# Performance work log

Measured on AMD Instinct MI355X. Metric: run time of the kernel, lower is better.

## Reference

```python
import jax, jax.numpy as jnp
import numpy as np

INPUT_DIM, HIDDEN_DIM, N_CLASSES = 512, 256, 2
TOP_RATIO, MIN_PATCHES, K_INST = 0.7, 128, 8
B, N = 4, 16384


def setup_inputs() -> dict:
    key = jax.random.key(0)
    ks = jax.random.split(key, 10)
    D, H, C = INPUT_DIM, HIDDEN_DIM, N_CLASSES
    s = lambda fan: 1.0 / np.sqrt(fan)
    return {
        "features": jax.random.normal(ks[0], (B, N, D), dtype=jnp.float32),
        # attention_net: Linear(D->H) (dropout is identity in eval)
        "Wa": jax.random.uniform(ks[1], (D, H), minval=-s(D), maxval=s(D), dtype=jnp.float32),
        "ba": jax.random.uniform(ks[2], (H,), minval=-s(D), maxval=s(D), dtype=jnp.float32),
        # per-class attention branches: Linear(H->1), stacked over classes
        "Wbr": jax.random.uniform(ks[3], (C, H), minval=-s(H), maxval=s(H), dtype=jnp.float32),
        "bbr": jax.random.uniform(ks[4], (C,), minval=-s(H), maxval=s(H), dtype=jnp.float32),
        # per-class instance classifiers: Linear(D->H) -> ReLU -> Linear(H->2)
        "W1": jax.random.uniform(ks[5], (C, D, H), minval=-s(D), maxval=s(D), dtype=jnp.float32),
        "b1": jax.random.uniform(ks[6], (C, H), minval=-s(D), maxval=s(D), dtype=jnp.float32),
        "W2": jax.random.uniform(ks[7], (C, H, 2), minval=-s(H), maxval=s(H), dtype=jnp.float32),
        "b2": jax.random.uniform(ks[8], (C, 2), minval=-s(H), maxval=s(H), dtype=jnp.float32),
    }


def reference(features, Wa, ba, Wbr, bbr, W1, b1, W2, b2):
    Bb, Nn, D = features.shape
    C = Wbr.shape[0]

    # ---- compute_attention ----
    h = jax.nn.relu(features @ Wa + ba)                       # (B,N,H)
    a_logits = jnp.einsum('bnh,ch->bcn', h, Wbr) + bbr[None, :, None]
    attn_all = jax.nn.softmax(a_logits, axis=-1)              # (B,C,N)
    combined = attn_all.mean(axis=1)                          # (B,N)

    # ---- per-sample top-k selection (k static under jit) ----
    k = min(max(int(Nn * TOP_RATIO), MIN_PATCHES), Nn)
    _, sel_idx = jax.lax.top_k(combined, k)                   # (B,k)
    sel_idx = jnp.sort(sel_idx, axis=-1)
    selected = jnp.take_along_axis(features, sel_idx[..., None], axis=1)  # (B,k,D)

    # ---- instance clustering loss (vectorized over B x C) ----
    kk = min(K_INST, Nn // 2)
    _, top_idx = jax.lax.top_k(attn_all, kk)                  # (B,C,kk)
    _, bot_idx = jax.lax.top_k(-attn_all, kk)                 # largest=False
    both_idx = jnp.concatenate([top_idx, bot_idx], axis=-1)   # (B,C,2kk)
    inst = features[jnp.arange(Bb)[:, None, None], both_idx]  # (B,C,2kk,D)
    h1 = jax.nn.relu(jnp.einsum('bckd,cdh->bckh', inst, W1) + b1[None, :, None, :])
    logits = jnp.einsum('bckh,cho->bcko', h1, W2) + b2[None, :, None, :]  # (B,C,2kk,2)
    labels = jnp.concatenate([jnp.ones(kk, jnp.int32), jnp.zeros(kk, jnp.int32)])
    logp = jax.nn.log_softmax(logits, axis=-1)
    ce = -jnp.take_along_axis(
        logp, jnp.broadcast_to(labels[None, None, :, None], (Bb, C, 2 * kk, 1)), axis=-1
    )[..., 0]                                                 # (B,C,2kk)
    cl_loss = ce.mean(axis=-1).sum() / (Bb * C)

    return selected, combined, sel_idx, cl_loss
```

## Files before the change

kernel.cpp:

```cpp
#include <hip/hip_runtime.h>

#define NB 4
#define NP 16384
#define DD 512
#define HH 256
#define CC 2
#define KSEL 11468
#define TOTP (NB*NP)
#define BCAP 4096

#define OFF_COMB (NB*KSEL*DD)
#define OFF_IDX  (OFF_COMB + NB*NP)
#define OFF_LOSS (OFF_IDX + NB*KSEL)

#define WS_ALOGIT 0
#define WS_ATTN   (NB*CC*NP)
#define WS_SELIDX (2*NB*CC*NP)
#define WS_MZ     (WS_SELIDX + NB*KSEL)
#define WS_BCNT   (WS_MZ + 16)
#define WS_BLIST  (WS_BCNT + 4)
#define WS_TOP16  (WS_BLIST + NB*BCAP)
#define WS_CE     (WS_TOP16 + 128)

typedef __attribute__((ext_vector_type(8))) short short8x;
typedef __attribute__((ext_vector_type(4))) float f32x4;

__device__ __forceinline__ unsigned short f2bf(float x){
  unsigned u = __float_as_uint(x);
  unsigned r = (u + 0x7FFFu + ((u >> 16) & 1u)) >> 16;
  return (unsigned short)r;
}

__global__ __launch_bounds__(256) void waconv_kernel(
    const float* __restrict__ Wa, unsigned short* __restrict__ WaT)
{
  __shared__ float tile[32][33];
  const int tx = threadIdx.x, ty = threadIdx.y;
  const int k0 = blockIdx.x * 32, n0 = blockIdx.y * 32;
  #pragma unroll
  for (int i=0;i<4;++i)
    tile[ty+8*i][tx] = Wa[(size_t)(k0+ty+8*i)*HH + n0 + tx];
  __syncthreads();
  #pragma unroll
  for (int i=0;i<4;++i)
    WaT[(size_t)(n0+ty+8*i)*DD + k0 + tx] = f2bf(tile[tx][ty+8*i]);
}

__global__ __launch_bounds__(512) void gemm_mfma_kernel(
    const float* __restrict__ feat, const unsigned short* __restrict__ WaT,
    const float* __restrict__ ba, const float* __restrict__ Wbr,
    const float* __restrict__ bbr, float* __restrict__ aL)
{
  __shared__ __attribute__((aligned(16))) unsigned char smem[65536];
  __shared__ float sBA[HH], sW0[HH], sW1[HH];
  unsigned char* sA = smem;
  unsigned char* sB = smem + 16384;

  const int tid  = threadIdx.x;
  const int lane = tid & 63;
  const int wid  = tid >> 6;
  const int wm = wid >> 2, wn = wid & 3;
  const int fr = lane & 15, fq = lane >> 4;
  const int p0 = blockIdx.x * 128;
  const float bb0 = bbr[0], bb1 = bbr[1];

  if (tid < HH){ sBA[tid] = ba[tid]; sW0[tid] = Wbr[tid]; sW1[tid] = Wbr[HH+tid]; }

  f32x4 acc[4][4];
  #pragma unroll
  for (int i=0;i<4;++i)
    #pragma unroll
    for (int j=0;j<4;++j)
      acc[i][j] = (f32x4){0.f,0.f,0.f,0.f};

  const int am = tid >> 2, akq = (tid & 3) * 16;
  const int bn = tid >> 1, bhf = tid & 1;

  for (int k0 = 0; k0 < DD; k0 += 64){
    __syncthreads();
    {
      const float4* src = reinterpret_cast<const float4*>(
          feat + (size_t)(p0 + am)*DD + k0 + akq);
      float4 v0 = src[0], v1 = src[1], v2 = src[2], v3 = src[3];
      unsigned short u[16];
      u[0]=f2bf(v0.x); u[1]=f2bf(v0.y); u[2]=f2bf(v0.z); u[3]=f2bf(v0.w);
      u[4]=f2bf(v1.x); u[5]=f2bf(v1.y); u[6]=f2bf(v1.z); u[7]=f2bf(v1.w);
      u[8]=f2bf(v2.x); u[9]=f2bf(v2.y); u[10]=f2bf(v2.z); u[11]=f2bf(v2.w);
      u[12]=f2bf(v3.x); u[13]=f2bf(v3.y); u[14]=f2bf(v3.z); u[15]=f2bf(v3.w);
      uint4 w0, w1;
      w0.x = (unsigned)u[0] | ((unsigned)u[1]<<16);
      w0.y = (unsigned)u[2] | ((unsigned)u[3]<<16);
      w0.z = (unsigned)u[4] | ((unsigned)u[5]<<16);
      w0.w = (unsigned)u[6] | ((unsigned)u[7]<<16);
      w1.x = (unsigned)u[8] | ((unsigned)u[9]<<16);
      w1.y = (unsigned)u[10] | ((unsigned)u[11]<<16);
      w1.z = (unsigned)u[12] | ((unsigned)u[13]<<16);
      w1.w = (unsigned)u[14] | ((unsigned)u[15]<<16);
      const int swz = (am & 7) << 4;
      *reinterpret_cast<uint4*>(sA + (((am*128) + akq*2) ^ swz)) = w0;
      *reinterpret_cast<uint4*>(sA + (((am*128) + akq*2 + 16) ^ swz)) = w1;
    }
    {
      const uint4* src = reinterpret_cast<const uint4*>(
          WaT + (size_t)bn*DD + k0 + bhf*32);
      uint4 q0 = src[0], q1 = src[1], q2 = src[2], q3 = src[3];
      const int swz = (bn & 7) << 4;
      const int base = bn*128 + bhf*64;
      *reinterpret_cast<uint4*>(sB + ((base     ) ^ swz)) = q0;
      *reinterpret_cast<uint4*>(sB + ((base + 16) ^ swz)) = q1;
      *reinterpret_cast<uint4*>(sB + ((base + 32) ^ swz)) = q2;
      *reinterpret_cast<uint4*>(sB + ((base + 48) ^ swz)) = q3;
    }
    __syncthreads();
    #pragma unroll
    for (int kf = 0; kf < 2; ++kf){
      short8x af[4], bf[4];
      #pragma unroll
      for (int mf = 0; mf < 4; ++mf){
        int m_loc = wm*64 + mf*16 + fr;
        int off = ((m_loc*128 + kf*64 + fq*16) ^ ((m_loc & 7) << 4));
        af[mf] = *reinterpret_cast<const short8x*>(sA + off);
      }
      #pragma unroll
      for (int nf = 0; nf < 4; ++nf){
        int n_loc = wn*64 + nf*16 + fr;
        int off = ((n_loc*128 + kf*64 + fq*16) ^ ((n_loc & 7) << 4));
        bf[nf] = *reinterpret_cast<const short8x*>(sB + off);
      }
      #pragma unroll
      for (int mf = 0; mf < 4; ++mf)
        #pragma unroll
        for (int nf = 0; nf < 4; ++nf)
          acc[mf][nf] = __builtin_amdgcn_mfma_f32_16x16x32_bf16(
              af[mf], bf[nf], acc[mf][nf], 0, 0, 0);
    }
  }
  __syncthreads();

  float* hS = reinterpret_cast<float*>(smem);
  #pragma unroll
  for (int mh = 0; mh < 2; ++mh){
    if (wm == mh){
      #pragma unroll
      for (int mf = 0; mf < 4; ++mf)
        #pragma unroll
        for (int nf = 0; nf < 4; ++nf)
          #pragma unroll
          for (int r = 0; r < 4; ++r){
            int row = mf*16 + fq*4 + r;
            int col = wn*64 + nf*16 + fr;
            hS[row*256 + col] = acc[mf][nf][r];
          }
    }
    __syncthreads();
    {
      const int row = tid >> 3, cg = tid & 7;
      float s0 = 0.f, s1 = 0.f;
      #pragma unroll
      for (int j = 0; j < 8; ++j){
        int col = cg*4 + j*32;
        float4 hv = *reinterpret_cast<const float4*>(&hS[row*256 + col]);
        float xs[4] = {hv.x, hv.y, hv.z, hv.w};
        #pragma unroll
        for (int u = 0; u < 4; ++u){
          int ccol = col + u;
          float x = fmaxf(xs[u] + sBA[ccol], 0.f);
          s0 += x * sW0[ccol];
          s1 += x * sW1[ccol];
        }
      }
      s0 += __shfl_xor(s0,1); s1 += __shfl_xor(s1,1);
      s0 += __shfl_xor(s0,2); s1 += __shfl_xor(s1,2);
      s0 += __shfl_xor(s0,4); s1 += __shfl_xor(s1,4);
      if (cg == 0){
        int p = p0 + mh*64 + row;
        int b = p >> 14, nl = p & (NP-1);
        aL[((size_t)b*CC + 0)*NP + nl] = s0 + bb0;
        aL[((size_t)b*CC + 1)*NP + nl] = s1 + bb1;
      }
    }
    __syncthreads();
  }
}

__global__ __launch_bounds__(1024) void softmax2_kernel(
    const float* __restrict__ aL, float* __restrict__ attn,
    float* __restrict__ comb, float* __restrict__ mz)
{
  __shared__ float  s_redf[16];
  __shared__ double s_redd[16];
  __shared__ float  s_m[2];
  __shared__ float  s_iz[2];
  const int tid = threadIdx.x;
  const int lane = tid & 63, wid = tid >> 6;
  const int b = blockIdx.x;

  #pragma unroll
  for (int c = 0; c < 2; ++c){
    const float* a = aL + ((size_t)b*CC + c)*NP;
    float m = -1e30f;
    for (int n = tid; n < NP; n += 1024) m = fmaxf(m, a[n]);
    #pragma unroll
    for (int off=1; off<64; off<<=1) m = fmaxf(m, __shfl_xor(m, off));
    if (lane==0) s_redf[wid] = m;
    __syncthreads();
    if (tid==0){ float mm=s_redf[0]; for(int w=1;w<16;++w) mm=fmaxf(mm,s_redf[w]); s_m[c]=mm; }
    __syncthreads();
    m = s_m[c];
    double ls = 0.0;
    for (int n = tid; n < NP; n += 1024) ls += (double)expf(a[n]-m);
    #pragma unroll
    for (int off=1; off<64; off<<=1) ls += __shfl_xor(ls, off);
    if (lane==0) s_redd[wid] = ls;
    __syncthreads();
    if (tid==0){ double t=0; for(int w=0;w<16;++w) t+=s_redd[w]; s_iz[c]=(float)(1.0/t); }
    __syncthreads();
  }
  const float m0 = s_m[0], iz0 = s_iz[0], m1 = s_m[1], iz1 = s_iz[1];
  const float* a0 = aL + ((size_t)b*CC + 0)*NP;
  const float* a1 = aL + ((size_t)b*CC + 1)*NP;
  float* o0 = attn + ((size_t)b*CC + 0)*NP;
  float* o1 = attn + ((size_t)b*CC + 1)*NP;
  float* oc = comb + (size_t)b*NP;
  for (int n = tid; n < NP; n += 1024){
    float e0 = expf(a0[n]-m0)*iz0;
    float e1 = expf(a1[n]-m1)*iz1;
    o0[n] = e0; o1[n] = e1; oc[n] = 0.5f*(e0+e1);
  }
  if (tid==0){ mz[b*4+0]=m0; mz[b*4+1]=iz0; mz[b*4+2]=m1; mz[b*4+3]=iz1; }
}

#define SKW 1028
__global__ __launch_bounds__(1024) void selT_kernel(
    const float* __restrict__ comb, int* __restrict__ bcnt,
    int* __restrict__ blist)
{
  __shared__ unsigned s_bits[16*SKW];
  __shared__ unsigned s_red[16];
  __shared__ unsigned s_bcast;
  __shared__ int s_cnt;
  const int tid = threadIdx.x;
  const int b = blockIdx.x;
  const int lane = tid & 63, wid = tid >> 6;
  const float* row = comb + (size_t)b*NP;
  for (int j=0;j<16;++j){
    int n = tid + j*1024;
    s_bits[(n & 15)*SKW + (n >> 4)] = __float_as_uint(row[n]);
  }
  if (tid==0) s_cnt = 0;
  __syncthreads();
  unsigned cur = 0;
  for (int bit=31; bit>=12; --bit){
    unsigned trial = cur | (1u<<bit);
    int c = 0;
    #pragma unroll
    for (int j=0;j<16;++j) c += (s_bits[j*SKW + tid] >= trial) ? 1 : 0;
    #pragma unroll
    for (int off=1; off<64; off<<=1) c += __shfl_xor(c, off);
    if (lane==0) s_red[wid] = (unsigned)c;
    __syncthreads();
    if (tid==0){ unsigned t=0; for(int w=0;w<16;++w) t+=s_red[w]; s_bcast=t; }
    __syncthreads();
    if (s_bcast >= KSEL) cur = trial;
    __syncthreads();
  }
  const float Tv = __uint_as_float(cur);
  const float lo = Tv*0.989f, hi = Tv*1.0115f;
  #pragma unroll
  for (int e=0;e<16;++e){
    float v = __uint_as_float(s_bits[e*SKW + tid]);
    if (v >= lo && v <= hi){
      int s = atomicAdd(&s_cnt, 1);
      if (s < BCAP) blist[b*BCAP + s] = tid*16 + e;
    }
  }
  __syncthreads();
  if (tid==0) bcnt[b] = (s_cnt < BCAP) ? s_cnt : BCAP;
}

__global__ __launch_bounds__(256) void recomp_kernel(
    const float* __restrict__ feat, const float* __restrict__ Wa,
    const float* __restrict__ ba, const float* __restrict__ Wbr,
    const float* __restrict__ bbr, const float* __restrict__ mz,
    const int* __restrict__ bcnt, const int* __restrict__ blist,
    float* __restrict__ comb)
{
  __shared__ float fS[DD];
  __shared__ float r0[4], r1[4];
  const int tid = threadIdx.x;
  const int b = blockIdx.x >> 12;
  const int s = blockIdx.x & (BCAP-1);
  if (s >= bcnt[b]) return;
  const int lane = tid & 63, wid = tid >> 6;
  const float m0 = mz[b*4+0], iz0 = mz[b*4+1], m1 = mz[b*4+2], iz1 = mz[b*4+3];
  const int n = blist[b*BCAP + s];
  if (tid < 128){
    float4 v = *reinterpret_cast<const float4*>(feat + ((size_t)b*NP + n)*DD + tid*4);
    *reinterpret_cast<float4*>(&fS[tid*4]) = v;
  }
  __syncthreads();
  float a0=0.f,a1=0.f,a2=0.f,a3=0.f;
  #pragma unroll 4
  for (int d=0; d<DD; d+=4){
    a0 += fS[d+0]*Wa[(size_t)(d+0)*HH + tid];
    a1 += fS[d+1]*Wa[(size_t)(d+1)*HH + tid];
    a2 += fS[d+2]*Wa[(size_t)(d+2)*HH + tid];
    a3 += fS[d+3]*Wa[(size_t)(d+3)*HH + tid];
  }
  float h = fmaxf((a0+a1)+(a2+a3) + ba[tid], 0.f);
  float p0 = h*Wbr[tid], p1 = h*Wbr[HH+tid];
  #pragma unroll
  for (int off=1; off<64; off<<=1){ p0+=__shfl_xor(p0,off); p1+=__shfl_xor(p1,off); }
  if (lane==0){ r0[wid]=p0; r1[wid]=p1; }
  __syncthreads();
  if (tid==0){
    float l0 = (r0[0]+r0[1])+(r0[2]+r0[3]) + bbr[0];
    float l1 = (r1[0]+r1[1])+(r1[2]+r1[3]) + bbr[1];
    comb[(size_t)b*NP + n] = 0.5f*(expf(l0-m0)*iz0 + expf(l1-m1)*iz1);
  }
}

__global__ __launch_bounds__(1024) void select_kernel(
    const float* __restrict__ comb, float* __restrict__ outIdxF,
    int* __restrict__ selIdx)
{
  __shared__ unsigned s_bits[16*SKW];
  __shared__ unsigned s_red[16];
  __shared__ unsigned s_scan[1024];
  __shared__ unsigned s_bcast;
  const int tid = threadIdx.x;
  const int b = blockIdx.x;
  const int lane = tid & 63, wid = tid >> 6;
  const float* row = comb + (size_t)b*NP;
  for (int j=0;j<16;++j){
    int n = tid + j*1024;
    s_bits[(n & 15)*SKW + (n >> 4)] = __float_as_uint(row[n]);
  }
  __syncthreads();
  unsigned cur = 0;
  for (int bit=31; bit>=0; --bit){
    unsigned trial = cur | (1u<<bit);
    int c = 0;
    #pragma unroll
    for (int j=0;j<16;++j) c += (s_bits[j*SKW + tid] >= trial) ? 1 : 0;
    #pragma unroll
    for (int off=1; off<64; off<<=1) c += __shfl_xor(c, off);
    if (lane==0) s_red[wid] = (unsigned)c;
    __syncthreads();
    if (tid==0){ unsigned t=0; for(int w=0;w<16;++w) t+=s_red[w]; s_bcast=t; }
    __syncthreads();
    if (s_bcast >= KSEL) cur = trial;
    __syncthreads();
  }
  const unsigned T = cur;
  {
    int c = 0;
    #pragma unroll
    for (int j=0;j<16;++j) c += (s_bits[j*SKW + tid] > T) ? 1 : 0;
    #pragma unroll
    for (int off=1; off<64; off<<=1) c += __shfl_xor(c, off);
    if (lane==0) s_red[wid] = (unsigned)c;
    __syncthreads();
    if (tid==0){ unsigned t=0; for(int w=0;w<16;++w) t+=s_red[w]; s_bcast=t; }
    __syncthreads();
  }
  const int extra = KSEL - (int)s_bcast;
  __syncthreads();
  int eqc=0;
  #pragma unroll
  for (int e=0;e<16;++e) eqc += (s_bits[e*SKW + tid]==T) ? 1 : 0;
  s_scan[tid]=(unsigned)eqc;
  __syncthreads();
  for (int off=1; off<1024; off<<=1){
    unsigned v = (tid>=off)? s_scan[tid-off] : 0u;
    __syncthreads();
    s_scan[tid]+=v;
    __syncthreads();
  }
  const int eqBase = (int)s_scan[tid] - eqc;
  __syncthreads();
  int eq=eqBase, sc=0;
  #pragma unroll
  for (int e=0;e<16;++e){
    unsigned v = s_bits[e*SKW + tid];
    if (v==T){ if (eq<extra) sc++; eq++; }
    else if (v>T) sc++;
  }
  s_scan[tid]=(unsigned)sc;
  __syncthreads();
  for (int off=1; off<1024; off<<=1){
    unsigned v = (tid>=off)? s_scan[tid-off] : 0u;
    __syncthreads();
    s_scan[tid]+=v;
    __syncthreads();
  }
  int pos = (int)s_scan[tid] - sc;
  eq=eqBase;
  #pragma unroll
  for (int e=0;e<16;++e){
    unsigned v = s_bits[e*SKW + tid];
    int f=0;
    if (v==T){ if (eq<extra) f=1; eq++; }
    else if (v>T) f=1;
    if (f){
      int n = tid*16 + e;
      outIdxF[(size_t)b*KSEL + pos] = (float)n;
      selIdx[(size_t)b*KSEL + pos] = n;
      pos++;
    }
  }
}

__global__ __launch_bounds__(256) void gather_kernel(
    const float* __restrict__ feat, const int* __restrict__ selIdx,
    float* __restrict__ outSel)
{
  const int tid = threadIdx.x;
  const int row = blockIdx.x*2 + (tid>>7);
  const int c4 = tid & 127;
  const int b = row / KSEL;
  const int idx = selIdx[row];
  const float4 v = *reinterpret_cast<const float4*>(feat + ((size_t)b*NP + idx)*DD + c4*4);
  *reinterpret_cast<float4*>(outSel + (size_t)row*DD + c4*4) = v;
}

__global__ __launch_bounds__(256) void top16_kernel(
    const float* __restrict__ attn, int* __restrict__ top16)
{
  __shared__ unsigned long long keys[2048];
  __shared__ unsigned long long red[4];
  __shared__ unsigned long long gkey;
  const int tid = threadIdx.x;
  const int bid = blockIdx.x;
  const int lane = tid & 63, wid = tid >> 6;
  const float* a = attn + (size_t)bid*NP;

  unsigned long long t8[8];
  #pragma unroll
  for (int i=0;i<8;++i) t8[i]=0ull;
  for (int j=0;j<64;++j){
    int n = tid + 256*j;
    unsigned long long key = ((unsigned long long)__float_as_uint(a[n])<<32) | (unsigned)(NP-1-n);
    if (key > t8[7]){
      t8[7]=key;
      #pragma unroll
      for (int i=7;i>0;--i){ if (t8[i]>t8[i-1]){ unsigned long long t=t8[i-1]; t8[i-1]=t8[i]; t8[i]=t; } }
    }
  }
  #pragma unroll
  for (int i=0;i<8;++i) keys[tid*8+i]=t8[i];
  __syncthreads();
  for (int pick=0; pick<8; ++pick){
    unsigned long long loc = 0ull;
    #pragma unroll
    for (int i=0;i<8;++i){ unsigned long long k=keys[tid*8+i]; loc = k>loc?k:loc; }
    #pragma unroll
    for (int off=1; off<64; off<<=1){ unsigned long long o=__shfl_xor(loc,off); loc=o>loc?o:loc; }
    if (lane==0) red[wid]=loc;
    __syncthreads();
    if (tid==0){
      unsigned long long m=red[0];
      for (int w=1;w<4;++w) m = red[w]>m?red[w]:m;
      gkey=m;
      top16[bid*16+pick] = NP-1-(int)(m & 0xFFFFFFFFull);
    }
    __syncthreads();
    unsigned long long g = gkey;
    #pragma unroll
    for (int i=0;i<8;++i) if (keys[tid*8+i]==g) keys[tid*8+i]=0ull;
    __syncthreads();
  }
  unsigned long long b8[8];
  #pragma unroll
  for (int i=0;i<8;++i) b8[i]=~0ull;
  for (int j=0;j<64;++j){
    int n = tid + 256*j;
    unsigned long long key = ((unsigned long long)__float_as_uint(a[n])<<32) | (unsigned)n;
    if (key < b8[7]){
      b8[7]=key;
      #pragma unroll
      for (int i=7;i>0;--i){ if (b8[i]<b8[i-1]){ unsigned long long t=b8[i-1]; b8[i-1]=b8[i]; b8[i]=t; } }
    }
  }
  __syncthreads();
  #pragma unroll
  for (int i=0;i<8;++i) keys[tid*8+i]=b8[i];
  __syncthreads();
  for (int pick=8; pick<16; ++pick){
    unsigned long long loc = ~0ull;
    #pragma unroll
    for (int i=0;i<8;++i){ unsigned long long k=keys[tid*8+i]; loc = k<loc?k:loc; }
    #pragma unroll
    for (int off=1; off<64; off<<=1){ unsigned long long o=__shfl_xor(loc,off); loc=o<loc?o:loc; }
    if (lane==0) red[wid]=loc;
    __syncthreads();
    if (tid==0){
      unsigned long long m=red[0];
      for (int w=1;w<4;++w) m = red[w]<m?red[w]:m;
      gkey=m;
      top16[bid*16+pick] = (int)(m & 0xFFFFFFFFull);
    }
    __syncthreads();
    unsigned long long g = gkey;
    #pragma unroll
    for (int i=0;i<8;++i) if (keys[tid*8+i]==g) keys[tid*8+i]=~0ull;
    __syncthreads();
  }
}

__global__ __launch_bounds__(256) void mlp_kernel(
    const float* __restrict__ feat, const float* __restrict__ W1,
    const float* __restrict__ b1, const float* __restrict__ W2,
    const float* __restrict__ b2, const int* __restrict__ top16,
    float* __restrict__ cews)
{
  __shared__ float fS[DD];
  __shared__ float r0[4], r1[4];
  const int tid = threadIdx.x;
  const int bid = blockIdx.x;
  const int r = bid & 15, c = (bid >> 4) & 1, b = bid >> 5;
  const int lane = tid & 63, wid = tid >> 6;
  const int gi = top16[(b*2+c)*16 + r];
  if (tid < 128){
    float4 v = *reinterpret_cast<const float4*>(feat + ((size_t)b*NP + gi)*DD + tid*4);
    *reinterpret_cast<float4*>(&fS[tid*4]) = v;
  }
  __syncthreads();
  const float* w1c = W1 + (size_t)c*DD*HH;
  float a0=0.f,a1=0.f,a2=0.f,a3=0.f;
  #pragma unroll 4
  for (int d=0; d<DD; d+=4){
    a0 += fS[d+0]*w1c[(size_t)(d+0)*HH + tid];
    a1 += fS[d+1]*w1c[(size_t)(d+1)*HH + tid];
    a2 += fS[d+2]*w1c[(size_t)(d+2)*HH + tid];
    a3 += fS[d+3]*w1c[(size_t)(d+3)*HH + tid];
  }
  float h = fmaxf((a0+a1)+(a2+a3) + b1[c*HH+tid], 0.f);
  float p0 = h*W2[(size_t)(c*HH+tid)*2 + 0];
  float p1 = h*W2[(size_t)(c*HH+tid)*2 + 1];
  #pragma unroll
  for (int off=1; off<64; off<<=1){ p0+=__shfl_xor(p0,off); p1+=__shfl_xor(p1,off); }
  if (lane==0){ r0[wid]=p0; r1[wid]=p1; }
  __syncthreads();
  if (tid==0){
    float l0 = (r0[0]+r0[1])+(r0[2]+r0[3]) + b2[c*2+0];
    float l1 = (r1[0]+r1[1])+(r1[2]+r1[3]) + b2[c*2+1];
    float mm = fmaxf(l0,l1);
    float lse = mm + logf(expf(l0-mm)+expf(l1-mm));
    float chosen = (r<8) ? l1 : l0;
    cews[bid] = lse - chosen;
  }
}

__global__ void loss_kernel(const float* __restrict__ cews, float* __restrict__ out_loss){
  if (threadIdx.x==0 && blockIdx.x==0){
    float s=0.f;
    for (int i=0;i<128;++i) s += cews[i];
    out_loss[0] = s / 128.0f;
  }
}

extern "C" void kernel_launch(void* const* d_in, const int* in_sizes, int n_in,
                              void* d_out, int out_size, void* d_ws, size_t ws_size,
                              hipStream_t stream) {
  const float* feat = (const float*)d_in[0];
  const float* Wa   = (const float*)d_in[1];
  const float* ba   = (const float*)d_in[2];
  const float* Wbr  = (const float*)d_in[3];
  const float* bbr  = (const float*)d_in[4];
  const float* W1   = (const float*)d_in[5];
  const float* b1   = (const float*)d_in[6];
  const float* W2   = (const float*)d_in[7];
  const float* b2   = (const float*)d_in[8];
  float* out = (float*)d_out;
  float* ws  = (float*)d_ws;

  float* a_logits = ws + WS_ALOGIT;
  float* attn     = ws + WS_ATTN;
  int*   selIdx   = (int*)(ws + WS_SELIDX);
  float* mz       = ws + WS_MZ;
  int*   bcnt     = (int*)(ws + WS_BCNT);
  int*   blist    = (int*)(ws + WS_BLIST);
  int*   top16    = (int*)(ws + WS_TOP16);
  float* cews     = ws + WS_CE;

  unsigned short* WaT = (unsigned short*)d_out;

  hipLaunchKernelGGL(waconv_kernel, dim3(DD/32, HH/32), dim3(32,8), 0, stream,
                     Wa, WaT);
  hipLaunchKernelGGL(gemm_mfma_kernel, dim3(TOTP/128), dim3(512), 0, stream,
                     feat, WaT, ba, Wbr, bbr, a_logits);
  hipLaunchKernelGGL(softmax2_kernel, dim3(NB), dim3(1024), 0, stream,
                     a_logits, attn, out + OFF_COMB, mz);
  hipLaunchKernelGGL(selT_kernel, dim3(NB), dim3(1024), 0, stream,
                     out + OFF_COMB, bcnt, blist);
  hipLaunchKernelGGL(recomp_kernel, dim3(NB*BCAP), dim3(256), 0, stream,
                     feat, Wa, ba, Wbr, bbr, mz, bcnt, blist, out + OFF_COMB);
  hipLaunchKernelGGL(select_kernel, dim3(NB), dim3(1024), 0, stream,
                     out + OFF_COMB, out + OFF_IDX, selIdx);
  hipLaunchKernelGGL(gather_kernel, dim3(NB*KSEL/2), dim3(256), 0, stream,
                     feat, selIdx, out);
  hipLaunchKernelGGL(top16_kernel, dim3(NB*CC), dim3(256), 0, stream,
                     attn, top16);
  hipLaunchKernelGGL(mlp_kernel, dim3(NB*CC*16), dim3(256), 0, stream,
                     feat, W1, b1, W2, b2, top16, cews);
  hipLaunchKernelGGL(loss_kernel, dim3(1), dim3(64), 0, stream,
                     cews, out + OFF_LOSS);
}
```

Baseline: 298.5 us.

## Split softmax stats across blocks, fuse normalization into threshold select, streamline top16

Softmax statistics now run with one block per (batch, class) row, giving 8 blocks instead of 4. Normalization and the combined-attention write are fused into the threshold-search kernel, so the comb row is no longer re-read. top16 now scans attention once with float4 loads, keeping top and bottom candidates together, and merges them with warp-level shuffles instead of repeated block-wide barrier rounds. This cuts launch-serial work and synchronization in small latency-bound kernels. The mz layout (m, iz per row) happens to match the old per-batch indexing.

```diff
diff --git a/kernel.cpp b/kernel.cpp
--- a/kernel.cpp
+++ b/kernel.cpp
@@ -183,57 +183,42 @@
   }
 }
 
-__global__ __launch_bounds__(1024) void softmax2_kernel(
-    const float* __restrict__ aL, float* __restrict__ attn,
-    float* __restrict__ comb, float* __restrict__ mz)
+__global__ __launch_bounds__(1024) void smstat_kernel(
+    const float* __restrict__ aL, float* __restrict__ mz)
 {
   __shared__ float  s_redf[16];
   __shared__ double s_redd[16];
-  __shared__ float  s_m[2];
-  __shared__ float  s_iz[2];
+  __shared__ float  s_max;
   const int tid = threadIdx.x;
   const int lane = tid & 63, wid = tid >> 6;
-  const int b = blockIdx.x;
-
-  #pragma unroll
-  for (int c = 0; c < 2; ++c){
-    const float* a = aL + ((size_t)b*CC + c)*NP;
-    float m = -1e30f;
-    for (int n = tid; n < NP; n += 1024) m = fmaxf(m, a[n]);
-    #pragma unroll
-    for (int off=1; off<64; off<<=1) m = fmaxf(m, __shfl_xor(m, off));
-    if (lane==0) s_redf[wid] = m;
-    __syncthreads();
-    if (tid==0){ float mm=s_redf[0]; for(int w=1;w<16;++w) mm=fmaxf(mm,s_redf[w]); s_m[c]=mm; }
-    __syncthreads();
-    m = s_m[c];
-    double ls = 0.0;
-    for (int n = tid; n < NP; n += 1024) ls += (double)expf(a[n]-m);
-    #pragma unroll
-    for (int off=1; off<64; off<<=1) ls += __shfl_xor(ls, off);
-    if (lane==0) s_redd[wid] = ls;
-    __syncthreads();
-    if (tid==0){ double t=0; for(int w=0;w<16;++w) t+=s_redd[w]; s_iz[c]=(float)(1.0/t); }
-    __syncthreads();
-  }
-  const float m0 = s_m[0], iz0 = s_iz[0], m1 = s_m[1], iz1 = s_iz[1];
-  const float* a0 = aL + ((size_t)b*CC + 0)*NP;
-  const float* a1 = aL + ((size_t)b*CC + 1)*NP;
-  float* o0 = attn + ((size_t)b*CC + 0)*NP;
-  float* o1 = attn + ((size_t)b*CC + 1)*NP;
-  float* oc = comb + (size_t)b*NP;
-  for (int n = tid; n < NP; n += 1024){
-    float e0 = expf(a0[n]-m0)*iz0;
-    float e1 = expf(a1[n]-m1)*iz1;
-    o0[n] = e0; o1[n] = e1; oc[n] = 0.5f*(e0+e1);
-  }
-  if (tid==0){ mz[b*4+0]=m0; mz[b*4+1]=iz0; mz[b*4+2]=m1; mz[b*4+3]=iz1; }
+  const int r = blockIdx.x;
+  const float* a = aL + (size_t)r*NP;
+  float m = -1e30f;
+  for (int n=tid; n<NP; n+=1024) m = fmaxf(m, a[n]);
+  #pragma unroll
+  for (int off=1; off<64; off<<=1) m = fmaxf(m, __shfl_xor(m, off));
+  if (lane==0) s_redf[wid]=m;
+  __syncthreads();
+  if (tid==0){ float mm=s_redf[0]; for(int w=1;w<16;++w) mm=fmaxf(mm,s_redf[w]); s_max=mm; }
+  __syncthreads();
+  m = s_max;
+  double ls = 0.0;
+  for (int n=tid;n<NP;n+=1024) ls += (double)expf(a[n]-m);
+  #pragma unroll
+  for (int off=1; off<64; off<<=1) ls += __shfl_xor(ls, off);
+  if (lane==0) s_redd[wid]=ls;
+  __syncthreads();
+  if (tid==0){
+    double t=0; for(int w=0;w<16;++w) t+=s_redd[w];
+    mz[r*2+0]=m; mz[r*2+1]=(float)(1.0/t);
+  }
 }
 
 #define SKW 1028
-__global__ __launch_bounds__(1024) void selT_kernel(
-    const float* __restrict__ comb, int* __restrict__ bcnt,
-    int* __restrict__ blist)
+__global__ __launch_bounds__(1024) void selTF_kernel(
+    const float* __restrict__ aL, const float* __restrict__ mz,
+    float* __restrict__ attn, float* __restrict__ comb,
+    int* __restrict__ bcnt, int* __restrict__ blist)
 {
   __shared__ unsigned s_bits[16*SKW];
   __shared__ unsigned s_red[16];
@@ -242,10 +227,20 @@
   const int tid = threadIdx.x;
   const int b = blockIdx.x;
   const int lane = tid & 63, wid = tid >> 6;
-  const float* row = comb + (size_t)b*NP;
+  const float m0 = mz[b*4+0], iz0 = mz[b*4+1], m1 = mz[b*4+2], iz1 = mz[b*4+3];
+  const float* a0 = aL + ((size_t)b*CC + 0)*NP;
+  const float* a1 = aL + ((size_t)b*CC + 1)*NP;
+  float* o0 = attn + ((size_t)b*CC + 0)*NP;
+  float* o1 = attn + ((size_t)b*CC + 1)*NP;
+  float* oc = comb + (size_t)b*NP;
   for (int j=0;j<16;++j){
     int n = tid + j*1024;
-    s_bits[(n & 15)*SKW + (n >> 4)] = __float_as_uint(row[n]);
+    float e0 = expf(a0[n]-m0)*iz0;
+    float e1 = expf(a1[n]-m1)*iz1;
+    o0[n]=e0; o1[n]=e1;
+    float cv = 0.5f*(e0+e1);
+    oc[n]=cv;
+    s_bits[(n & 15)*SKW + (n >> 4)] = __float_as_uint(cv);
   }
   if (tid==0) s_cnt = 0;
   __syncthreads();
@@ -427,84 +422,83 @@
 __global__ __launch_bounds__(256) void top16_kernel(
     const float* __restrict__ attn, int* __restrict__ top16)
 {
-  __shared__ unsigned long long keys[2048];
-  __shared__ unsigned long long red[4];
-  __shared__ unsigned long long gkey;
+  __shared__ unsigned long long wkT[4][8];
+  __shared__ unsigned long long wkB[4][8];
   const int tid = threadIdx.x;
   const int bid = blockIdx.x;
   const int lane = tid & 63, wid = tid >> 6;
   const float* a = attn + (size_t)bid*NP;
 
-  unsigned long long t8[8];
-  #pragma unroll
-  for (int i=0;i<8;++i) t8[i]=0ull;
-  for (int j=0;j<64;++j){
-    int n = tid + 256*j;
-    unsigned long long key = ((unsigned long long)__float_as_uint(a[n])<<32) | (unsigned)(NP-1-n);
-    if (key > t8[7]){
-      t8[7]=key;
+  unsigned long long t8[8], b8[8];
+  #pragma unroll
+  for (int i=0;i<8;++i){ t8[i]=0ull; b8[i]=~0ull; }
+
+  for (int j=0;j<16;++j){
+    const int n4 = tid + 256*j;
+    const float4 v = *reinterpret_cast<const float4*>(a + 4*n4);
+    const float xs[4] = {v.x, v.y, v.z, v.w};
+    #pragma unroll
+    for (int q=0;q<4;++q){
+      const int n = 4*n4 + q;
+      const unsigned vb = __float_as_uint(xs[q]);
+      unsigned long long kt = ((unsigned long long)vb<<32) | (unsigned)(NP-1-n);
+      if (kt > t8[7]){
+        t8[7]=kt;
+        #pragma unroll
+        for (int i=7;i>0;--i){ if (t8[i]>t8[i-1]){ unsigned long long t=t8[i-1]; t8[i-1]=t8[i]; t8[i]=t; } }
+      }
+      unsigned long long kb = ((unsigned long long)vb<<32) | (unsigned)n;
+      if (kb < b8[7]){
+        b8[7]=kb;
+        #pragma unroll
+        for (int i=7;i>0;--i){ if (b8[i]<b8[i-1]){ unsigned long long t=b8[i-1]; b8[i-1]=b8[i]; b8[i]=t; } }
+      }
+    }
+  }
+
+  #pragma unroll
+  for (int pick=0; pick<8; ++pick){
+    unsigned long long loc = t8[0];
+    #pragma unroll
+    for (int i=1;i<8;++i) loc = t8[i]>loc ? t8[i] : loc;
+    #pragma unroll
+    for (int off=1; off<64; off<<=1){ unsigned long long o=__shfl_xor(loc,off); loc=o>loc?o:loc; }
+    if (lane==0) wkT[wid][pick]=loc;
+    #pragma unroll
+    for (int i=0;i<8;++i) if (t8[i]==loc) t8[i]=0ull;
+  }
+  #pragma unroll
+  for (int pick=0; pick<8; ++pick){
+    unsigned long long loc = b8[0];
+    #pragma unroll
+    for (int i=1;i<8;++i) loc = b8[i]<loc ? b8[i] : loc;
+    #pragma unroll
+    for (int off=1; off<64; off<<=1){ unsigned long long o=__shfl_xor(loc,off); loc=o<loc?o:loc; }
+    if (lane==0) wkB[wid][pick]=loc;
+    #pragma unroll
+    for (int i=0;i<8;++i) if (b8[i]==loc) b8[i]=~0ull;
+  }
+  __syncthreads();
+
+  if (wid==0){
+    unsigned long long k = (lane<32) ? wkT[lane>>3][lane&7] : 0ull;
+    #pragma unroll
+    for (int pick=0; pick<8; ++pick){
+      unsigned long long loc = k;
       #pragma unroll
-      for (int i=7;i>0;--i){ if (t8[i]>t8[i-1]){ unsigned long long t=t8[i-1]; t8[i-1]=t8[i]; t8[i]=t; } }
-    }
-  }
-  #pragma unroll
-  for (int i=0;i<8;++i) keys[tid*8+i]=t8[i];
-  __syncthreads();
-  for (int pick=0; pick<8; ++pick){
-    unsigned long long loc = 0ull;
-    #pragma unroll
-    for (int i=0;i<8;++i){ unsigned long long k=keys[tid*8+i]; loc = k>loc?k:loc; }
-    #pragma unroll
-    for (int off=1; off<64; off<<=1){ unsigned long long o=__shfl_xor(loc,off); loc=o>loc?o:loc; }
-    if (lane==0) red[wid]=loc;
-    __syncthreads();
-    if (tid==0){
-      unsigned long long m=red[0];
-      for (int w=1;w<4;++w) m = red[w]>m?red[w]:m;
-      gkey=m;
-      top16[bid*16+pick] = NP-1-(int)(m & 0xFFFFFFFFull);
-    }
-    __syncthreads();
-    unsigned long long g = gkey;
-    #pragma unroll
-    for (int i=0;i<8;++i) if (keys[tid*8+i]==g) keys[tid*8+i]=0ull;
-    __syncthreads();
-  }
-  unsigned long long b8[8];
-  #pragma unroll
-  for (int i=0;i<8;++i) b8[i]=~0ull;
-  for (int j=0;j<64;++j){
-    int n = tid + 256*j;
-    unsigned long long key = ((unsigned long long)__float_as_uint(a[n])<<32) | (unsigned)n;
-    if (key < b8[7]){
-      b8[7]=key;
+      for (int off=1; off<64; off<<=1){ unsigned long long o=__shfl_xor(loc,off); loc=o>loc?o:loc; }
+      if (k==loc) k=0ull;
+      if (lane==0) top16[bid*16+pick] = NP-1-(int)(loc & 0xFFFFFFFFull);
+    }
+    unsigned long long kb = (lane<32) ? wkB[lane>>3][lane&7] : ~0ull;
+    #pragma unroll
+    for (int pick=0; pick<8; ++pick){
+      unsigned long long loc = kb;
       #pragma unroll
-      for (int i=7;i>0;--i){ if (b8[i]<b8[i-1]){ unsigned long long t=b8[i-1]; b8[i-1]=b8[i]; b8[i]=t; } }
-    }
-  }
-  __syncthreads();
-  #pragma unroll
-  for (int i=0;i<8;++i) keys[tid*8+i]=b8[i];
-  __syncthreads();
-  for (int pick=8; pick<16; ++pick){
-    unsigned long long loc = ~0ull;
-    #pragma unroll
-    for (int i=0;i<8;++i){ unsigned long long k=keys[tid*8+i]; loc = k<loc?k:loc; }
-    #pragma unroll
-    for (int off=1; off<64; off<<=1){ unsigned long long o=__shfl_xor(loc,off); loc=o<loc?o:loc; }
-    if (lane==0) red[wid]=loc;
-    __syncthreads();
-    if (tid==0){
-      unsigned long long m=red[0];
-      for (int w=1;w<4;++w) m = red[w]<m?red[w]:m;
-      gkey=m;
-      top16[bid*16+pick] = (int)(m & 0xFFFFFFFFull);
-    }
-    __syncthreads();
-    unsigned long long g = gkey;
-    #pragma unroll
-    for (int i=0;i<8;++i) if (keys[tid*8+i]==g) keys[tid*8+i]=~0ull;
-    __syncthreads();
+      for (int off=1; off<64; off<<=1){ unsigned long long o=__shfl_xor(loc,off); loc=o<loc?o:loc; }
+      if (kb==loc) kb=~0ull;
+      if (lane==0) top16[bid*16+8+pick] = (int)(loc & 0xFFFFFFFFull);
+    }
   }
 }
 
@@ -590,10 +584,10 @@
                      Wa, WaT);
   hipLaunchKernelGGL(gemm_mfma_kernel, dim3(TOTP/128), dim3(512), 0, stream,
                      feat, WaT, ba, Wbr, bbr, a_logits);
-  hipLaunchKernelGGL(softmax2_kernel, dim3(NB), dim3(1024), 0, stream,
-                     a_logits, attn, out + OFF_COMB, mz);
-  hipLaunchKernelGGL(selT_kernel, dim3(NB), dim3(1024), 0, stream,
-                     out + OFF_COMB, bcnt, blist);
+  hipLaunchKernelGGL(smstat_kernel, dim3(NB*CC), dim3(1024), 0, stream,
+                     a_logits, mz);
+  hipLaunchKernelGGL(selTF_kernel, dim3(NB), dim3(1024), 0, stream,
+                     a_logits, mz, attn, out + OFF_COMB, bcnt, blist);
   hipLaunchKernelGGL(recomp_kernel, dim3(NB*BCAP), dim3(256), 0, stream,
                      feat, Wa, ba, Wbr, bbr, mz, bcnt, blist, out + OFF_COMB);
   hipLaunchKernelGGL(select_kernel, dim3(NB), dim3(1024), 0, stream,
```

Result: faster. 283.7 us (-5.0%).
